# Kernel optimization log

Hardware: AMD Instinct MI355X
Metric: run time of the kernel (lower is better)

## Reference

```python
import jax, jax.numpy as jnp
import numpy as np

L_LAYERS = 4
N_HEAD = 16
D_MODEL = 1024
D_K = 64
D_V = 64
D_HID = 4096
D_OUT = 10000
SEQ = 512
BATCH = 16
MASK_RATE = 0.15
LN_EPS = 1e-5


def sinusoid_table(n_position, model_size):
    pos = np.arange(n_position)[:, None]
    hid = np.arange(model_size)[None, :]
    angle = pos / np.power(10000, 2 * (hid // 2) / model_size)
    tab = np.array(angle)
    tab[:, 0::2] = np.sin(tab[:, 0::2])
    tab[:, 1::2] = np.cos(tab[:, 1::2])
    return jnp.asarray(tab, dtype=jnp.float32)


def layer_norm(x, w, b):
    mu = jnp.mean(x, axis=-1, keepdims=True)
    var = jnp.mean(jnp.square(x - mu), axis=-1, keepdims=True)
    return (x - mu) * jax.lax.rsqrt(var + LN_EPS) * w + b


def setup_inputs() -> dict:
    key = jax.random.key(0)
    ks = jax.random.split(key, 32)
    s = 0.02
    inp = {
        "x": jax.random.normal(ks[0], (SEQ, BATCH, D_MODEL), dtype=jnp.float32),
        "rnd": jax.random.uniform(ks[1], (BATCH, SEQ), dtype=jnp.float32),
        "posi": sinusoid_table(SEQ, D_MODEL),
        "ln0_w": jnp.ones((D_MODEL,), jnp.float32),
        "ln0_b": jnp.zeros((D_MODEL,), jnp.float32),
        # stacked per-layer params [L, ...]
        "Wq": jax.random.normal(ks[2], (L_LAYERS, N_HEAD * D_K, D_MODEL), jnp.float32) * np.sqrt(2.0 / (D_MODEL + D_K)),
        "bq": jnp.zeros((L_LAYERS, N_HEAD * D_K), jnp.float32),
        "Wk": jax.random.normal(ks[3], (L_LAYERS, N_HEAD * D_K, D_MODEL), jnp.float32) * np.sqrt(2.0 / (D_MODEL + D_K)),
        "bk": jnp.zeros((L_LAYERS, N_HEAD * D_K), jnp.float32),
        "Wv": jax.random.normal(ks[4], (L_LAYERS, N_HEAD * D_V, D_MODEL), jnp.float32) * np.sqrt(2.0 / (D_MODEL + D_V)),
        "bv": jnp.zeros((L_LAYERS, N_HEAD * D_V), jnp.float32),
        "Wfc": jax.random.normal(ks[5], (L_LAYERS, D_MODEL, N_HEAD * D_V), jnp.float32) * s,
        "bfc": jnp.zeros((L_LAYERS, D_MODEL), jnp.float32),
        "ln1_w": jnp.ones((L_LAYERS, D_MODEL), jnp.float32),
        "ln1_b": jnp.zeros((L_LAYERS, D_MODEL), jnp.float32),
        "W1": jax.random.normal(ks[6], (L_LAYERS, D_HID, D_MODEL), jnp.float32) * s,
        "b1": jnp.zeros((L_LAYERS, D_HID), jnp.float32),
        "W2": jax.random.normal(ks[7], (L_LAYERS, D_MODEL, D_HID), jnp.float32) * s,
        "b2": jnp.zeros((L_LAYERS, D_MODEL), jnp.float32),
        "ln2_w": jnp.ones((L_LAYERS, D_MODEL), jnp.float32),
        "ln2_b": jnp.zeros((L_LAYERS, D_MODEL), jnp.float32),
        "Wo": jax.random.normal(ks[8], (D_OUT, D_MODEL), jnp.float32) * s,
        "bo": jnp.zeros((D_OUT,), jnp.float32),
    }
    return inp


def reference(x, rnd, posi, ln0_w, ln0_b, Wq, bq, Wk, bk, Wv, bv, Wfc, bfc,
              ln1_w, ln1_b, W1, b1, W2, b2, ln2_w, ln2_b, Wo, bo):
    scale = 1.0 / np.sqrt(D_K)
    # [length, batch, d] -> [batch, length, d]
    h = jnp.transpose(x, (1, 0, 2))
    # random input masking: keep where rnd > mask_rate
    keep = (rnd > MASK_RATE).astype(h.dtype)  # [B, S]
    h = h * keep[:, :, None]
    enc = layer_norm(h, ln0_w, ln0_b) + posi[None, :, :]

    for l in range(L_LAYERS):
        residual = enc
        q = (enc @ Wq[l].T + bq[l]).reshape(BATCH, SEQ, N_HEAD, D_K)
        k = (enc @ Wk[l].T + bk[l]).reshape(BATCH, SEQ, N_HEAD, D_K)
        v = (enc @ Wv[l].T + bv[l]).reshape(BATCH, SEQ, N_HEAD, D_V)
        attn = jnp.einsum('bqhd,bkhd->bhqk', q, k) * scale
        attn = jax.nn.softmax(attn, axis=-1)
        out = jnp.einsum('bhqk,bkhd->bqhd', attn, v).reshape(BATCH, SEQ, N_HEAD * D_V)
        out = out @ Wfc[l].T + bfc[l]
        enc = layer_norm(out + residual, ln1_w[l], ln1_b[l])
        # position-wise FFN (conv1d kernel=1 == per-token linear)
        ff = jax.nn.relu(enc @ W1[l].T + b1[l]) @ W2[l].T + b2[l]
        enc = layer_norm(ff + enc, ln2_w[l], ln2_b[l])

    logits = enc @ Wo.T + bo  # [B, S, D_OUT]
    out = jax.nn.log_softmax(logits, axis=-1)
    return jnp.transpose(out, (1, 0, 2))  # [S, B, D_OUT]
```

## Files before the change

kernel.cpp:

```cpp
#include <hip/hip_runtime.h>
#include <cstdint>

typedef unsigned short u16;
typedef unsigned int u32;
typedef __attribute__((ext_vector_type(8))) short vs8;
typedef __attribute__((ext_vector_type(4))) short vs4;
typedef __attribute__((ext_vector_type(4))) float vf4;
typedef __attribute__((ext_vector_type(4))) float f32x4;

#define NLAYER 4
#define SEQ 512
#define BATCH 16
#define DM 1024
#define NTOK 8192
#define DOUT 10000
#define DOUTP 10240

static __device__ __forceinline__ u16 f2bf(float f) {
    u32 u = __float_as_uint(f);
    return (u16)((u + 0x7FFFu + ((u >> 16) & 1u)) >> 16);
}
static __device__ __forceinline__ float bf2f(u16 h) { return __uint_as_float((u32)h << 16); }

static __device__ __forceinline__ void gload16(const void* g, void* l) {
    __builtin_amdgcn_global_load_lds(
        (const __attribute__((address_space(1))) u32*)(uintptr_t)g,
        (__attribute__((address_space(3))) u32*)(u32)(uintptr_t)l, 16, 0, 0);
}

template <int BM, bool RELU, bool OUTBF, bool NTST>
__global__ __launch_bounds__(512, 1) void gemm8p(const u16* __restrict__ A, const u16* __restrict__ Bw,
                                                 const float* __restrict__ bias, void* __restrict__ Cv,
                                                 int N, int K, int nMt, int nNt)
{
    constexpr int LA = BM / 128;
    constexpr int LB = 2;
    constexpr int WCNT = 2 * (LA + LB);
    constexpr int MR = BM / 32;
    constexpr int MR2 = MR / 2;

    __shared__ __align__(16) u16 lds[2 * 2 * BM * 32 + 2 * 2 * 256 * 32];
    u16* As = lds;
    u16* Bs = lds + 2 * 2 * BM * 32;

    const int t = threadIdx.x;
    const int wid = t >> 6, lane = t & 63;
    const int lr = lane & 15, lg = lane >> 4;
    const int wr = wid >> 2, wc = wid & 3;
    const int wrb = wr * (BM / 2), wcb = wc * 64;
    const int slot8 = (lg ^ ((lr >> 1) & 3)) * 8;

    const int nwg = nMt * nNt;
    const int orig = blockIdx.x;
    const int q8 = nwg >> 3, r8 = nwg & 7;
    const int xcd = orig & 7, idx = orig >> 3;
    const int wg = ((xcd < r8) ? xcd * (q8 + 1) : r8 * (q8 + 1) + (xcd - r8) * q8) + idx;
    const int GN = 8;
    const int gsz = GN * nMt;
    const int grp = wg / gsz;
    const int rem = wg - grp * gsz;
    const int gw = min(GN, nNt - grp * GN);
    const int mt = rem / gw;
    const int nt = grp * GN + (rem - mt * gw);
    const size_t m0 = (size_t)mt * BM;
    const size_t n0 = (size_t)nt * 256;

    const int srow = wid * 16 + (lane >> 2);
    const int scg = (lane & 3) ^ ((lane >> 3) & 3);
    const u16* gA = A + (m0 + srow) * (size_t)K + scg * 8;
    const u16* gB = Bw + (n0 + srow) * (size_t)K + scg * 8;

    auto stageA = [&](int b, int kh, int kt) {
#pragma unroll
        for (int i = 0; i < LA; ++i)
            gload16(gA + (size_t)i * 128 * K + kt + kh * 32,
                    &As[(((b << 1) + kh) * BM + (i * 8 + wid) * 16) * 32]);
    };
    auto stageB = [&](int b, int kh, int kt) {
#pragma unroll
        for (int i = 0; i < LB; ++i)
            gload16(gB + (size_t)i * 128 * K + kt + kh * 32,
                    &Bs[(((b << 1) + kh) * 256 + (i * 8 + wid) * 16) * 32]);
    };
    auto ldA = [&](int i, int kk, int b) -> vs8 {
        return *(const vs8*)&As[(((b << 1) + kk) * BM + wrb + i * 16 + lr) * 32 + slot8];
    };
    auto ldB = [&](int j, int kk, int b) -> vs8 {
        return *(const vs8*)&Bs[(((b << 1) + kk) * 256 + wcb + j * 16 + lr) * 32 + slot8];
    };

    f32x4 acc[MR][4];
#pragma unroll
    for (int i = 0; i < MR; ++i)
#pragma unroll
        for (int j = 0; j < 4; ++j) acc[i][j] = (f32x4){0.f, 0.f, 0.f, 0.f};

    const int NT = K >> 6;

    stageA(0, 0, 0); stageB(0, 0, 0);
    stageA(0, 1, 0); stageB(0, 1, 0);
    const int kt1 = (NT > 1 ? 64 : 0);
    stageA(1, 0, kt1); stageB(1, 0, kt1);
    if constexpr (WCNT == 8) asm volatile("s_waitcnt vmcnt(8)" ::: "memory");
    else                     asm volatile("s_waitcnt vmcnt(6)" ::: "memory");
    __builtin_amdgcn_s_barrier();

    for (int tt = 0; tt < NT; ++tt) {
        const int buf = tt & 1;
        const int ktn = min(tt + 1, NT - 1) << 6;
        const int ktn2 = min(tt + 2, NT - 1) << 6;
        vs8 af[MR2], bf[4];

#pragma unroll
        for (int j = 0; j < 4; ++j) bf[j] = ldB(j, 0, buf);
#pragma unroll
        for (int i = 0; i < MR2; ++i) af[i] = ldA(i, 0, buf);
        stageA(buf ^ 1, 1, ktn);
        __builtin_amdgcn_s_barrier();
        asm volatile("s_waitcnt lgkmcnt(0)" ::: "memory");
        __builtin_amdgcn_sched_barrier(0);
        __builtin_amdgcn_s_setprio(1);
#pragma unroll
        for (int i = 0; i < MR2; ++i)
#pragma unroll
            for (int j = 0; j < 4; ++j)
                acc[i][j] = __builtin_amdgcn_mfma_f32_16x16x32_bf16(bf[j], af[i], acc[i][j], 0, 0, 0);
        __builtin_amdgcn_s_setprio(0);
        __builtin_amdgcn_s_barrier();

#pragma unroll
        for (int i = 0; i < MR2; ++i) af[i] = ldA(MR2 + i, 0, buf);
        stageB(buf ^ 1, 1, ktn);
        __builtin_amdgcn_s_barrier();
        asm volatile("s_waitcnt lgkmcnt(0)" ::: "memory");
        __builtin_amdgcn_sched_barrier(0);
        __builtin_amdgcn_s_setprio(1);
#pragma unroll
        for (int i = 0; i < MR2; ++i)
#pragma unroll
            for (int j = 0; j < 4; ++j)
                acc[MR2 + i][j] = __builtin_amdgcn_mfma_f32_16x16x32_bf16(bf[j], af[i], acc[MR2 + i][j], 0, 0, 0);
        __builtin_amdgcn_s_setprio(0);
        if constexpr (WCNT == 8) asm volatile("s_waitcnt vmcnt(8)" ::: "memory");
        else                     asm volatile("s_waitcnt vmcnt(6)" ::: "memory");
        __builtin_amdgcn_s_barrier();

#pragma unroll
        for (int j = 0; j < 4; ++j) bf[j] = ldB(j, 1, buf);
#pragma unroll
        for (int i = 0; i < MR2; ++i) af[i] = ldA(i, 1, buf);
        stageA(buf, 0, ktn2);
        __builtin_amdgcn_s_barrier();
        asm volatile("s_waitcnt lgkmcnt(0)" ::: "memory");
        __builtin_amdgcn_sched_barrier(0);
        __builtin_amdgcn_s_setprio(1);
#pragma unroll
        for (int i = 0; i < MR2; ++i)
#pragma unroll
            for (int j = 0; j < 4; ++j)
                acc[i][j] = __builtin_amdgcn_mfma_f32_16x16x32_bf16(bf[j], af[i], acc[i][j], 0, 0, 0);
        __builtin_amdgcn_s_setprio(0);
        __builtin_amdgcn_s_barrier();

#pragma unroll
        for (int i = 0; i < MR2; ++i) af[i] = ldA(MR2 + i, 1, buf);
        stageB(buf, 0, ktn2);
        __builtin_amdgcn_s_barrier();
        asm volatile("s_waitcnt lgkmcnt(0)" ::: "memory");
        __builtin_amdgcn_sched_barrier(0);
        __builtin_amdgcn_s_setprio(1);
#pragma unroll
        for (int i = 0; i < MR2; ++i)
#pragma unroll
            for (int j = 0; j < 4; ++j)
                acc[MR2 + i][j] = __builtin_amdgcn_mfma_f32_16x16x32_bf16(bf[j], af[i], acc[MR2 + i][j], 0, 0, 0);
        __builtin_amdgcn_s_setprio(0);
        if constexpr (WCNT == 8) asm volatile("s_waitcnt vmcnt(8)" ::: "memory");
        else                     asm volatile("s_waitcnt vmcnt(6)" ::: "memory");
        __builtin_amdgcn_s_barrier();
    }

    asm volatile("s_waitcnt vmcnt(0)" ::: "memory");

#pragma unroll
    for (int i = 0; i < MR; ++i) {
        const size_t cm = m0 + wrb + 16 * i + lr;
#pragma unroll
        for (int j = 0; j < 4; ++j) {
            const size_t cn = n0 + wcb + 16 * j + lg * 4;
            const vf4 bv4 = *(const vf4*)&bias[cn];
            f32x4 v = acc[i][j];
#pragma unroll
            for (int r = 0; r < 4; ++r) {
                v[r] += bv4[r];
                if (RELU) v[r] = fmaxf(v[r], 0.f);
            }
            if (OUTBF) {
                vs4 o;
#pragma unroll
                for (int r = 0; r < 4; ++r) o[r] = (short)f2bf(v[r]);
                vs4* dst = (vs4*)&((u16*)Cv)[cm * (size_t)N + cn];
                if (NTST) __builtin_nontemporal_store(o, dst);
                else      *dst = o;
            } else {
                vf4* dst = (vf4*)&((float*)Cv)[cm * (size_t)N + cn];
                if (NTST) __builtin_nontemporal_store(v, dst);
                else      *dst = v;
            }
        }
    }
}

__global__ __launch_bounds__(256) void vtrans_k(const u16* __restrict__ vb, u16* __restrict__ vt, int ldv)
{
    __shared__ u16 tile[64][80];
    const int t = threadIdx.x;
    const int bh = blockIdx.x >> 3, st = blockIdx.x & 7;
    const int b = bh >> 4, h = bh & 15;
    const int s0 = st * 64;
    {
        const int s = t >> 2, d0 = (t & 3) * 16;
        const vs8* src = (const vs8*)(vb + ((size_t)(b * 512 + s0 + s)) * ldv + h * 64 + d0);
        *(vs8*)&tile[s][d0] = src[0];
        *(vs8*)&tile[s][d0 + 8] = src[1];
    }
    __syncthreads();
    {
        const int d = t >> 2, r0 = (t & 3) * 16;
        u16 tmp[16];
#pragma unroll
        for (int i = 0; i < 16; ++i) tmp[i] = tile[r0 + i][d];
        vs8* dst = (vs8*)(vt + ((size_t)bh * 64 + d) * 512 + s0 + r0);
        dst[0] = *(const vs8*)&tmp[0];
        dst[1] = *(const vs8*)&tmp[8];
    }
}

__global__ __launch_bounds__(256) void attn_k(const u16* __restrict__ qb, const u16* __restrict__ kb,
                                              const u16* __restrict__ vtb, u16* __restrict__ ob, int ldq)
{
    __shared__ float Sl[32 * 512];
    const int t = threadIdx.x;
    const int wid = t >> 6, lane = t & 63;
    const int lr = lane & 15, lg = lane >> 4;
    const int bh = blockIdx.x >> 4, qt = blockIdx.x & 15;
    const int b = bh >> 4, h = bh & 15;
    const int q0 = qt * 32;

    vs8 aq[2][2];
#pragma unroll
    for (int i2 = 0; i2 < 2; ++i2)
#pragma unroll
        for (int kk = 0; kk < 2; ++kk)
            aq[i2][kk] = *(const vs8*)(qb + ((size_t)(b * 512 + q0 + 16 * i2 + lr)) * ldq + h * 64 + kk * 32 + lg * 8);

    f32x4 sa[2][8];
#pragma unroll
    for (int i2 = 0; i2 < 2; ++i2)
#pragma unroll
        for (int j = 0; j < 8; ++j) sa[i2][j] = (f32x4){0.f, 0.f, 0.f, 0.f};

#pragma unroll
    for (int j = 0; j < 8; ++j) {
        const int col = 128 * wid + 16 * j + lr;
#pragma unroll
        for (int kk = 0; kk < 2; ++kk) {
            vs8 bk = *(const vs8*)(kb + ((size_t)(b * 512 + col)) * ldq + h * 64 + kk * 32 + lg * 8);
#pragma unroll
            for (int i2 = 0; i2 < 2; ++i2)
                sa[i2][j] = __builtin_amdgcn_mfma_f32_16x16x32_bf16(aq[i2][kk], bk, sa[i2][j], 0, 0, 0);
        }
    }
#pragma unroll
    for (int i2 = 0; i2 < 2; ++i2)
#pragma unroll
        for (int j = 0; j < 8; ++j)
#pragma unroll
            for (int r = 0; r < 4; ++r)
                Sl[(16 * i2 + lg * 4 + r) * 512 + 128 * wid + 16 * j + lr] = sa[i2][j][r] * 0.125f;
    __syncthreads();

    {
        const int row = t >> 3, seg = t & 7;
        float v[64];
        float m = -3.0e38f;
#pragma unroll
        for (int i = 0; i < 64; ++i) {
            const int c = seg * 64 + ((i + 8 * row + seg) & 63);
            v[i] = Sl[row * 512 + c];
            m = fmaxf(m, v[i]);
        }
        m = fmaxf(m, __shfl_xor(m, 1));
        m = fmaxf(m, __shfl_xor(m, 2));
        m = fmaxf(m, __shfl_xor(m, 4));
        float s = 0.f;
#pragma unroll
        for (int i = 0; i < 64; ++i) { v[i] = __expf(v[i] - m); s += v[i]; }
        s += __shfl_xor(s, 1);
        s += __shfl_xor(s, 2);
        s += __shfl_xor(s, 4);
        const float inv = 1.f / s;
        u16* P = (u16*)Sl;
#pragma unroll
        for (int i = 0; i < 64; ++i) {
            const int c = seg * 64 + ((i + 8 * row + seg) & 63);
            P[row * 1024 + c] = f2bf(v[i] * inv);
        }
    }
    __syncthreads();

    const int rt = wid >> 1, ct0 = (wid & 1) * 2;
    f32x4 oa[2];
    oa[0] = (f32x4){0.f, 0.f, 0.f, 0.f};
    oa[1] = (f32x4){0.f, 0.f, 0.f, 0.f};
    const u16* P = (const u16*)Sl;
#pragma unroll
    for (int kt = 0; kt < 16; ++kt) {
        vs8 pa = *(const vs8*)(P + (16 * rt + lr) * 1024 + kt * 32 + lg * 8);
#pragma unroll
        for (int c = 0; c < 2; ++c) {
            const int col = (ct0 + c) * 16 + lr;
            vs8 bv = *(const vs8*)(vtb + ((size_t)bh * 64 + col) * 512 + kt * 32 + lg * 8);
            oa[c] = __builtin_amdgcn_mfma_f32_16x16x32_bf16(bv, pa, oa[c], 0, 0, 0);
        }
    }
#pragma unroll
    for (int c = 0; c < 2; ++c) {
        const int qq = q0 + 16 * rt + lr;
        const int d0c = h * 64 + (ct0 + c) * 16 + lg * 4;
        vs4 o;
#pragma unroll
        for (int r = 0; r < 4; ++r) o[r] = (short)f2bf(oa[c][r]);
        *(vs4*)&ob[((size_t)b * 512 + qq) * 1024 + d0c] = o;
    }
}

__global__ __launch_bounds__(256) void embed_k(const float* __restrict__ x, const float* __restrict__ rnd,
                                               const float* __restrict__ posi, const float* __restrict__ w,
                                               const float* __restrict__ bb, float* __restrict__ outf,
                                               u16* __restrict__ outb)
{
    const int tok = blockIdx.x;
    const int b = tok >> 9, s = tok & 511;
    const int t = threadIdx.x;
    const float keep = rnd[tok] > 0.15f ? 1.f : 0.f;
    vf4 xv = ((const vf4*)(x + ((size_t)s * 16 + b) * 1024))[t];
    xv *= keep;
    float s1 = xv[0] + xv[1] + xv[2] + xv[3];
    float s2 = xv[0] * xv[0] + xv[1] * xv[1] + xv[2] * xv[2] + xv[3] * xv[3];
#pragma unroll
    for (int mk = 1; mk < 64; mk <<= 1) { s1 += __shfl_xor(s1, mk); s2 += __shfl_xor(s2, mk); }
    __shared__ float red[8];
    if ((t & 63) == 0) { red[t >> 6] = s1; red[4 + (t >> 6)] = s2; }
    __syncthreads();
    s1 = red[0] + red[1] + red[2] + red[3];
    s2 = red[4] + red[5] + red[6] + red[7];
    const float mu = s1 * (1.f / 1024.f);
    const float var = s2 * (1.f / 1024.f) - mu * mu;
    const float rs = rsqrtf(var + 1e-5f);
    vf4 wv = ((const vf4*)w)[t];
    vf4 bv = ((const vf4*)bb)[t];
    vf4 pv = ((const vf4*)(posi + (size_t)s * 1024))[t];
    vf4 y;
    vs4 yb;
#pragma unroll
    for (int c = 0; c < 4; ++c) {
        y[c] = (xv[c] - mu) * rs * wv[c] + bv[c] + pv[c];
        yb[c] = (short)f2bf(y[c]);
    }
    ((vf4*)(outf + (size_t)tok * 1024))[t] = y;
    *(vs4*)(outb + (size_t)tok * 1024 + t * 4) = yb;
}

__global__ __launch_bounds__(256) void add_ln_k(const float* __restrict__ x, const float* __restrict__ resid,
                                                const float* __restrict__ w, const float* __restrict__ bb,
                                                float* __restrict__ outf, u16* __restrict__ outb)
{
    const size_t row = blockIdx.x;
    const int t = threadIdx.x;
    vf4 xv = ((const vf4*)(x + row * 1024))[t];
    vf4 rv = ((const vf4*)(resid + row * 1024))[t];
    xv += rv;
    float s1 = xv[0] + xv[1] + xv[2] + xv[3];
    float s2 = xv[0] * xv[0] + xv[1] * xv[1] + xv[2] * xv[2] + xv[3] * xv[3];
#pragma unroll
    for (int mk = 1; mk < 64; mk <<= 1) { s1 += __shfl_xor(s1, mk); s2 += __shfl_xor(s2, mk); }
    __shared__ float red[8];
    if ((t & 63) == 0) { red[t >> 6] = s1; red[4 + (t >> 6)] = s2; }
    __syncthreads();
    s1 = red[0] + red[1] + red[2] + red[3];
    s2 = red[4] + red[5] + red[6] + red[7];
    const float mu = s1 * (1.f / 1024.f);
    const float var = s2 * (1.f / 1024.f) - mu * mu;
    const float rs = rsqrtf(var + 1e-5f);
    vf4 wv = ((const vf4*)w)[t];
    vf4 bv = ((const vf4*)bb)[t];
    vf4 y;
    vs4 yb;
#pragma unroll
    for (int c = 0; c < 4; ++c) {
        y[c] = (xv[c] - mu) * rs * wv[c] + bv[c];
        yb[c] = (short)f2bf(y[c]);
    }
    ((vf4*)(outf + row * 1024))[t] = y;
    *(vs4*)(outb + row * 1024 + t * 4) = yb;
}

__global__ __launch_bounds__(256) void logsm_k(const u16* __restrict__ lgts, float* __restrict__ out)
{
    const int tok = blockIdx.x;
    const int b = tok >> 9, s = tok & 511;
    const int t = threadIdx.x;
    const u16* row = lgts + (size_t)tok * DOUTP;
    float v[40];
    float m = -3.0e38f;
#pragma unroll
    for (int i = 0; i < 40; ++i) {
        const int c = t + 256 * i;
        v[i] = (c < DOUT) ? bf2f(row[c]) : -3.0e38f;
        m = fmaxf(m, v[i]);
    }
#pragma unroll
    for (int mk = 1; mk < 64; mk <<= 1) m = fmaxf(m, __shfl_xor(m, mk));
    __shared__ float red[8];
    if ((t & 63) == 0) red[t >> 6] = m;
    __syncthreads();
    m = fmaxf(fmaxf(red[0], red[1]), fmaxf(red[2], red[3]));
    float sum = 0.f;
#pragma unroll
    for (int i = 0; i < 40; ++i) sum += __expf(v[i] - m);
#pragma unroll
    for (int mk = 1; mk < 64; mk <<= 1) sum += __shfl_xor(sum, mk);
    if ((t & 63) == 0) red[4 + (t >> 6)] = sum;
    __syncthreads();
    sum = red[4] + red[5] + red[6] + red[7];
    const float ls = m + __logf(sum);
    float* orow = out + ((size_t)s * 16 + b) * DOUT;
#pragma unroll
    for (int i = 0; i < 40; ++i) {
        const int c = t + 256 * i;
        if (c < DOUT) __builtin_nontemporal_store(v[i] - ls, &orow[c]);
    }
}

__global__ void conv_k(const float* __restrict__ src, u16* __restrict__ dst, int n4)
{
    const int i = blockIdx.x * 256 + threadIdx.x;
    if (i >= n4) return;
    vf4 v = ((const vf4*)src)[i];
    vs4 o;
#pragma unroll
    for (int c = 0; c < 4; ++c) o[c] = (short)f2bf(v[c]);
    ((vs4*)dst)[i] = o;
}

__global__ void convq_k(const float* __restrict__ src, u16* __restrict__ dst, int n4, int perl4,
                        int dstl4, int off4)
{
    const int i = blockIdx.x * 256 + threadIdx.x;
    if (i >= n4) return;
    const int l = i / perl4, r = i - l * perl4;
    vf4 v = ((const vf4*)src)[i];
    vs4 o;
#pragma unroll
    for (int c = 0; c < 4; ++c) o[c] = (short)f2bf(v[c]);
    ((vs4*)dst)[(size_t)l * dstl4 + off4 + r] = o;
}

__global__ void biasq_k(const float* __restrict__ bq, const float* __restrict__ bk,
                        const float* __restrict__ bv, float* __restrict__ dst)
{
    const int i = blockIdx.x * 256 + threadIdx.x;
    const int l2 = i / 3072, c = i - l2 * 3072;
    float v;
    if (c < 1024) v = bq[l2 * 1024 + c];
    else if (c < 2048) v = bk[l2 * 1024 + c - 1024];
    else v = bv[l2 * 1024 + c - 2048];
    dst[i] = v;
}

__global__ void padwo_k(const float* __restrict__ src, u16* __restrict__ dst)
{
    const int i = blockIdx.x * 256 + threadIdx.x;
    const size_t e = (size_t)i * 4;
    const int r = (int)(e >> 10);
    vs4 o;
    if (r < DOUT) {
        vf4 v = *(const vf4*)(src + (size_t)r * 1024 + (e & 1023));
#pragma unroll
        for (int c = 0; c < 4; ++c) o[c] = (short)f2bf(v[c]);
    } else {
        o[0] = o[1] = o[2] = o[3] = 0;
    }
    *(vs4*)(dst + e) = o;
}

__global__ void padbo_k(const float* __restrict__ src, float* __restrict__ dst)
{
    const int i = blockIdx.x * 256 + threadIdx.x;
    if (i < DOUTP) dst[i] = (i < DOUT) ? src[i] : 0.f;
}

extern "C" void kernel_launch(void* const* d_in, const int* in_sizes, int n_in,
                              void* d_out, int out_size, void* d_ws, size_t ws_size,
                              hipStream_t stream)
{
    (void)in_sizes; (void)n_in; (void)out_size; (void)ws_size;
    const float* x     = (const float*)d_in[0];
    const float* rnd   = (const float*)d_in[1];
    const float* posi  = (const float*)d_in[2];
    const float* ln0_w = (const float*)d_in[3];
    const float* ln0_b = (const float*)d_in[4];
    const float* Wq    = (const float*)d_in[5];
    const float* bq    = (const float*)d_in[6];
    const float* Wk    = (const float*)d_in[7];
    const float* bk    = (const float*)d_in[8];
    const float* Wv    = (const float*)d_in[9];
    const float* bv    = (const float*)d_in[10];
    const float* Wfc   = (const float*)d_in[11];
    const float* bfc   = (const float*)d_in[12];
    const float* ln1_w = (const float*)d_in[13];
    const float* ln1_b = (const float*)d_in[14];
    const float* W1    = (const float*)d_in[15];
    const float* b1    = (const float*)d_in[16];
    const float* W2    = (const float*)d_in[17];
    const float* b2    = (const float*)d_in[18];
    const float* ln2_w = (const float*)d_in[19];
    const float* ln2_b = (const float*)d_in[20];
    const float* Wo    = (const float*)d_in[21];
    const float* bo    = (const float*)d_in[22];

    const size_t l1e = 1024 * 1024;
    const size_t l2e = 4096 * 1024;
    const size_t l3e = 3072 * 1024;

    char* p = (char*)d_ws;
    size_t off = 0;
    auto take = [&](size_t bytes) {
        char* r = p + off;
        off += (bytes + 255) & ~(size_t)255;
        return r;
    };
    u16*   Wqkv_b = (u16*)take(NLAYER * l3e * 2);
    u16*   Wfc_b  = (u16*)take(NLAYER * l1e * 2);
    u16*   W1_b   = (u16*)take(NLAYER * l2e * 2);
    u16*   W2_b   = (u16*)take(NLAYER * l2e * 2);
    u16*   Wo_b   = (u16*)take((size_t)DOUTP * DM * 2);
    float* bqkv_p = (float*)take(NLAYER * 3072 * 4);
    float* bo_p   = (float*)take(DOUTP * 4);
    float* enc_f  = (float*)take((size_t)NTOK * DM * 4);
    u16*   enc_b  = (u16*)take((size_t)NTOK * DM * 2);
    char*  pool   = take((size_t)NTOK * DOUTP * 2);
    u16*   qkv_b  = (u16*)(pool);
    u16*   vt_b   = (u16*)(pool + 50331648);
    u16*   attn_b = (u16*)(pool + 67108864);
    float* fc_f   = (float*)(pool);
    u16*   ff_b   = (u16*)(pool);
    float* ff2_f  = (float*)(pool + 67108864);
    u16*   lgt_b  = (u16*)(pool);

    const dim3 blk(256);
    int n4;
    n4 = (int)(NLAYER * l1e / 4);
    convq_k<<<(n4 + 255) / 256, blk, 0, stream>>>(Wq, Wqkv_b, n4, 262144, 786432, 0);
    convq_k<<<(n4 + 255) / 256, blk, 0, stream>>>(Wk, Wqkv_b, n4, 262144, 786432, 262144);
    convq_k<<<(n4 + 255) / 256, blk, 0, stream>>>(Wv, Wqkv_b, n4, 262144, 786432, 524288);
    conv_k<<<(n4 + 255) / 256, blk, 0, stream>>>(Wfc, Wfc_b, n4);
    n4 = (int)(NLAYER * l2e / 4);
    conv_k<<<(n4 + 255) / 256, blk, 0, stream>>>(W1, W1_b, n4);
    conv_k<<<(n4 + 255) / 256, blk, 0, stream>>>(W2, W2_b, n4);
    padwo_k<<<(DOUTP * DM / 4) / 256, blk, 0, stream>>>(Wo, Wo_b);
    padbo_k<<<40, blk, 0, stream>>>(bo, bo_p);
    biasq_k<<<48, blk, 0, stream>>>(bq, bk, bv, bqkv_p);

    embed_k<<<NTOK, blk, 0, stream>>>(x, rnd, posi, ln0_w, ln0_b, enc_f, enc_b);

    for (int l = 0; l < NLAYER; ++l) {
        gemm8p<256, false, true, false><<<384, 512, 0, stream>>>(enc_b, Wqkv_b + l * l3e, bqkv_p + l * 3072,
                                                                 qkv_b, 3072, 1024, 32, 12);
        vtrans_k<<<2048, blk, 0, stream>>>(qkv_b + 2048, vt_b, 3072);
        attn_k<<<4096, blk, 0, stream>>>(qkv_b, qkv_b + 1024, vt_b, attn_b, 3072);
        gemm8p<128, false, false, false><<<256, 512, 0, stream>>>(attn_b, Wfc_b + l * l1e, bfc + l * 1024,
                                                                  fc_f, 1024, 1024, 64, 4);
        add_ln_k<<<NTOK, blk, 0, stream>>>(fc_f, enc_f, ln1_w + l * 1024, ln1_b + l * 1024, enc_f, enc_b);
        gemm8p<256, true, true, false><<<512, 512, 0, stream>>>(enc_b, W1_b + l * l2e, b1 + l * 4096,
                                                                ff_b, 4096, 1024, 32, 16);
        gemm8p<128, false, false, false><<<256, 512, 0, stream>>>(ff_b, W2_b + l * l2e, b2 + l * 1024,
                                                                  ff2_f, 1024, 4096, 64, 4);
        add_ln_k<<<NTOK, blk, 0, stream>>>(ff2_f, enc_f, ln2_w + l * 1024, ln2_b + l * 1024, enc_f, enc_b);
    }

    gemm8p<256, false, true, true><<<1280, 512, 0, stream>>>(enc_b, Wo_b, bo_p, lgt_b, DOUTP, 1024, 32, 40);
    logsm_k<<<NTOK, blk, 0, stream>>>(lgt_b, (float*)d_out);
}
```

Baseline: 2.157 ms.

## Keep residual stream and GEMM outputs in bf16, drop fp32 copies

Removes the fp32 residual buffer and makes the Wfc/W2 GEMMs write bf16 instead of fp32, so add+LayerNorm reads and writes bf16 only. This halves the memory traffic of those GEMM epilogues and the LayerNorm kernels, and drops the duplicate fp32 writes. It also removes the nontemporal store path on the logits GEMM. The cost is precision: residual accumulation across layers now happens in bf16, which adds rounding error.

```diff
diff --git a/kernel.cpp b/kernel.cpp
--- a/kernel.cpp
+++ b/kernel.cpp
@@ -28,7 +28,7 @@
         (__attribute__((address_space(3))) u32*)(u32)(uintptr_t)l, 16, 0, 0);
 }
 
-template <int BM, bool RELU, bool OUTBF, bool NTST>
+template <int BM, bool RELU, bool OUTBF>
 __global__ __launch_bounds__(512, 1) void gemm8p(const u16* __restrict__ A, const u16* __restrict__ Bw,
                                                  const float* __restrict__ bias, void* __restrict__ Cv,
                                                  int N, int K, int nMt, int nNt)
@@ -199,13 +199,9 @@
                 vs4 o;
 #pragma unroll
                 for (int r = 0; r < 4; ++r) o[r] = (short)f2bf(v[r]);
-                vs4* dst = (vs4*)&((u16*)Cv)[cm * (size_t)N + cn];
-                if (NTST) __builtin_nontemporal_store(o, dst);
-                else      *dst = o;
+                *(vs4*)&((u16*)Cv)[cm * (size_t)N + cn] = o;
             } else {
-                vf4* dst = (vf4*)&((float*)Cv)[cm * (size_t)N + cn];
-                if (NTST) __builtin_nontemporal_store(v, dst);
-                else      *dst = v;
+                *(vf4*)&((float*)Cv)[cm * (size_t)N + cn] = v;
             }
         }
     }
@@ -337,8 +333,7 @@
 
 __global__ __launch_bounds__(256) void embed_k(const float* __restrict__ x, const float* __restrict__ rnd,
                                                const float* __restrict__ posi, const float* __restrict__ w,
-                                               const float* __restrict__ bb, float* __restrict__ outf,
-                                               u16* __restrict__ outb)
+                                               const float* __restrict__ bb, u16* __restrict__ outb)
 {
     const int tok = blockIdx.x;
     const int b = tok >> 9, s = tok & 511;
@@ -361,26 +356,24 @@
     vf4 wv = ((const vf4*)w)[t];
     vf4 bv = ((const vf4*)bb)[t];
     vf4 pv = ((const vf4*)(posi + (size_t)s * 1024))[t];
-    vf4 y;
     vs4 yb;
 #pragma unroll
-    for (int c = 0; c < 4; ++c) {
-        y[c] = (xv[c] - mu) * rs * wv[c] + bv[c] + pv[c];
-        yb[c] = (short)f2bf(y[c]);
-    }
-    ((vf4*)(outf + (size_t)tok * 1024))[t] = y;
+    for (int c = 0; c < 4; ++c)
+        yb[c] = (short)f2bf((xv[c] - mu) * rs * wv[c] + bv[c] + pv[c]);
     *(vs4*)(outb + (size_t)tok * 1024 + t * 4) = yb;
 }
 
-__global__ __launch_bounds__(256) void add_ln_k(const float* __restrict__ x, const float* __restrict__ resid,
+__global__ __launch_bounds__(256) void add_ln_k(const u16* x, const u16* resid,
                                                 const float* __restrict__ w, const float* __restrict__ bb,
-                                                float* __restrict__ outf, u16* __restrict__ outb)
+                                                u16* out)
 {
     const size_t row = blockIdx.x;
     const int t = threadIdx.x;
-    vf4 xv = ((const vf4*)(x + row * 1024))[t];
-    vf4 rv = ((const vf4*)(resid + row * 1024))[t];
-    xv += rv;
+    const vs4 xv4 = *(const vs4*)(x + row * 1024 + t * 4);
+    const vs4 rv4 = *(const vs4*)(resid + row * 1024 + t * 4);
+    float xv[4];
+#pragma unroll
+    for (int c = 0; c < 4; ++c) xv[c] = bf2f((u16)xv4[c]) + bf2f((u16)rv4[c]);
     float s1 = xv[0] + xv[1] + xv[2] + xv[3];
     float s2 = xv[0] * xv[0] + xv[1] * xv[1] + xv[2] * xv[2] + xv[3] * xv[3];
 #pragma unroll
@@ -393,17 +386,13 @@
     const float mu = s1 * (1.f / 1024.f);
     const float var = s2 * (1.f / 1024.f) - mu * mu;
     const float rs = rsqrtf(var + 1e-5f);
-    vf4 wv = ((const vf4*)w)[t];
-    vf4 bv = ((const vf4*)bb)[t];
-    vf4 y;
+    const vf4 wv = ((const vf4*)w)[t];
+    const vf4 bv = ((const vf4*)bb)[t];
     vs4 yb;
 #pragma unroll
-    for (int c = 0; c < 4; ++c) {
-        y[c] = (xv[c] - mu) * rs * wv[c] + bv[c];
-        yb[c] = (short)f2bf(y[c]);
-    }
-    ((vf4*)(outf + row * 1024))[t] = y;
-    *(vs4*)(outb + row * 1024 + t * 4) = yb;
+    for (int c = 0; c < 4; ++c)
+        yb[c] = (short)f2bf((xv[c] - mu) * rs * wv[c] + bv[c]);
+    *(vs4*)(out + row * 1024 + t * 4) = yb;
 }
 
 __global__ __launch_bounds__(256) void logsm_k(const u16* __restrict__ lgts, float* __restrict__ out)
@@ -548,15 +537,14 @@
     u16*   Wo_b   = (u16*)take((size_t)DOUTP * DM * 2);
     float* bqkv_p = (float*)take(NLAYER * 3072 * 4);
     float* bo_p   = (float*)take(DOUTP * 4);
-    float* enc_f  = (float*)take((size_t)NTOK * DM * 4);
     u16*   enc_b  = (u16*)take((size_t)NTOK * DM * 2);
     char*  pool   = take((size_t)NTOK * DOUTP * 2);
     u16*   qkv_b  = (u16*)(pool);
     u16*   vt_b   = (u16*)(pool + 50331648);
     u16*   attn_b = (u16*)(pool + 67108864);
-    float* fc_f   = (float*)(pool);
+    u16*   fc_b   = (u16*)(pool);
     u16*   ff_b   = (u16*)(pool);
-    float* ff2_f  = (float*)(pool + 67108864);
+    u16*   ff2_b  = (u16*)(pool + 67108864);
     u16*   lgt_b  = (u16*)(pool);
 
     const dim3 blk(256);
@@ -573,23 +561,23 @@
     padbo_k<<<40, blk, 0, stream>>>(bo, bo_p);
     biasq_k<<<48, blk, 0, stream>>>(bq, bk, bv, bqkv_p);
 
-    embed_k<<<NTOK, blk, 0, stream>>>(x, rnd, posi, ln0_w, ln0_b, enc_f, enc_b);
+    embed_k<<<NTOK, blk, 0, stream>>>(x, rnd, posi, ln0_w, ln0_b, enc_b);
 
     for (int l = 0; l < NLAYER; ++l) {
-        gemm8p<256, false, true, false><<<384, 512, 0, stream>>>(enc_b, Wqkv_b + l * l3e, bqkv_p + l * 3072,
-                                                                 qkv_b, 3072, 1024, 32, 12);
+        gemm8p<256, false, true><<<384, 512, 0, stream>>>(enc_b, Wqkv_b + l * l3e, bqkv_p + l * 3072,
+                                                          qkv_b, 3072, 1024, 32, 12);
         vtrans_k<<<2048, blk, 0, stream>>>(qkv_b + 2048, vt_b, 3072);
         attn_k<<<4096, blk, 0, stream>>>(qkv_b, qkv_b + 1024, vt_b, attn_b, 3072);
-        gemm8p<128, false, false, false><<<256, 512, 0, stream>>>(attn_b, Wfc_b + l * l1e, bfc + l * 1024,
-                                                                  fc_f, 1024, 1024, 64, 4);
-        add_ln_k<<<NTOK, blk, 0, stream>>>(fc_f, enc_f, ln1_w + l * 1024, ln1_b + l * 1024, enc_f, enc_b);
-        gemm8p<256, true, true, false><<<512, 512, 0, stream>>>(enc_b, W1_b + l * l2e, b1 + l * 4096,
-                                                                ff_b, 4096, 1024, 32, 16);
-        gemm8p<128, false, false, false><<<256, 512, 0, stream>>>(ff_b, W2_b + l * l2e, b2 + l * 1024,
-                                                                  ff2_f, 1024, 4096, 64, 4);
-        add_ln_k<<<NTOK, blk, 0, stream>>>(ff2_f, enc_f, ln2_w + l * 1024, ln2_b + l * 1024, enc_f, enc_b);
-    }
-
-    gemm8p<256, false, true, true><<<1280, 512, 0, stream>>>(enc_b, Wo_b, bo_p, lgt_b, DOUTP, 1024, 32, 40);
+        gemm8p<128, false, true><<<256, 512, 0, stream>>>(attn_b, Wfc_b + l * l1e, bfc + l * 1024,
+                                                          fc_b, 1024, 1024, 64, 4);
+        add_ln_k<<<NTOK, blk, 0, stream>>>(fc_b, enc_b, ln1_w + l * 1024, ln1_b + l * 1024, enc_b);
+        gemm8p<256, true, true><<<512, 512, 0, stream>>>(enc_b, W1_b + l * l2e, b1 + l * 4096,
+                                                         ff_b, 4096, 1024, 32, 16);
+        gemm8p<128, false, true><<<256, 512, 0, stream>>>(ff_b, W2_b + l * l2e, b2 + l * 1024,
+                                                          ff2_b, 1024, 4096, 64, 4);
+        add_ln_k<<<NTOK, blk, 0, stream>>>(ff2_b, enc_b, ln2_w + l * 1024, ln2_b + l * 1024, enc_b);
+    }
+
+    gemm8p<256, false, true><<<1280, 512, 0, stream>>>(enc_b, Wo_b, bo_p, lgt_b, DOUTP, 1024, 32, 40);
     logsm_k<<<NTOK, blk, 0, stream>>>(lgt_b, (float*)d_out);
 }
```

Result: faster. 2.022 ms (-6.3%).
